# Performance work log

Measured on AMD Instinct MI355X. Metric: run time of the kernel, lower is better.

Reference implementation:

```python
import jax, jax.numpy as jnp
import numpy as np

B, C, N = 512, 4, 24
D, H, L, DFF = 512, 8, 4, 2048
D2, D4 = D // 2, D // 4


def _ln(x, g, b):
    m = x.mean(-1, keepdims=True)
    v = ((x - m) ** 2).mean(-1, keepdims=True)
    return (x - m) / jnp.sqrt(v + 1e-5) * g + b


def setup_inputs():
    key = jax.random.key(0)
    ks = iter(jax.random.split(key, 80))
    def glorot(shape):
        fi, fo = shape[-2], shape[-1]
        return jax.random.normal(next(ks), shape, jnp.float32) * np.float32(np.sqrt(2.0 / (fi + fo)))
    z = lambda shape: jnp.zeros(shape, jnp.float32)
    o = lambda shape: jnp.ones(shape, jnp.float32)
    inp = {
        'encoded_features': jax.random.normal(next(ks), (B, C, D), jnp.float32),
        'original_keypoints': jax.random.normal(next(ks), (B, C, N, 2), jnp.float32),
        'depth_map': jax.random.uniform(next(ks), (B, C, N), jnp.float32),
        'occlusion_mask': jax.random.bernoulli(next(ks), 0.7, (B, C, N)),
        'kp_emb': jax.random.normal(next(ks), (N, D), jnp.float32) * 0.02,
        'view_emb': jax.random.normal(next(ks), (C, D), jnp.float32) * 0.02,
        'Wq': glorot((L, D, D)), 'bq': z((L, D)),
        'Wk': glorot((L, D, D)), 'bk': z((L, D)),
        'Wv': glorot((L, D, D)), 'bv': z((L, D)),
        'Wo': glorot((L, D, D)), 'bo': z((L, D)),
        'ln1_g': o((L, D)), 'ln1_b': z((L, D)),
        'ln2_g': o((L, D)), 'ln2_b': z((L, D)),
        'ffn_w1': glorot((L, D, DFF)), 'ffn_b1': z((L, DFF)),
        'ffn_w2': glorot((L, DFF, D)), 'ffn_b2': z((L, D)),
        'pred_w1': glorot((D, D2)), 'pred_b1': z((D2,)),
        'pred_w2': glorot((D2, D4)), 'pred_b2': z((D4,)),
        'pred_w3': glorot((D4, 2)), 'pred_b3': z((2,)),
        'de_w1': glorot((1, D4)), 'de_b1': z((D4,)),
        'de_w2': glorot((D4, D2)), 'de_b2': z((D2,)),
        'mp_w': glorot((D + D2, D)), 'mp_b': z((D,)),
        'dp_w1': glorot((D, D2)), 'dp_b1': z((D2,)),
        'dp_w2': glorot((D2, D4)), 'dp_b2': z((D4,)),
        'dp_w3': glorot((D4, 1)), 'dp_b3': z((1,)),
        'conf_w': glorot((D, 1)), 'conf_b': z((1,)),
    }
    return inp


def _forward(encoded_features, original_keypoints, depth_map, kp_emb, view_emb,
             Wq, bq, Wk, bk, Wv, bv, Wo, bo, ln1_g, ln1_b, ln2_g, ln2_b,
             ffn_w1, ffn_b1, ffn_w2, ffn_b2, pred_w1, pred_b1, pred_w2, pred_b2,
             pred_w3, pred_b3, de_w1, de_b1, de_w2, de_b2, mp_w, mp_b,
             dp_w1, dp_b1, dp_w2, dp_b2, dp_w3, dp_b3, conf_w, conf_b,
             occlusion_mask):
    occluded = ~occlusion_mask  # (B,C,N) True = needs inpainting
    # Vectorized replacement for the nested B*C ragged depth loop:
    # encode every depth scalar, masked mean over visible keypoints per (b,c).
    d_enc = jax.nn.gelu(depth_map[..., None] @ de_w1 + de_b1) @ de_w2 + de_b2  # (B,C,N,D2)
    vis = occlusion_mask[..., None].astype(jnp.float32)
    cnt = vis.sum(2)  # (B,C,1)
    depth_feat = jnp.where(cnt > 0, (d_enc * vis).sum(2) / jnp.maximum(cnt, 1.0), 0.0)
    # NOTE: faithful to source — `memory` is projected but the attention layers
    # consume encoded_features directly, so this is dead w.r.t. outputs.
    _memory = jnp.concatenate([encoded_features, depth_feat], -1) @ mp_w + mp_b

    # Dense query set over all (c,n); occluded positions selected at the end
    # (same math as the nonzero/gather version, jit-friendly fixed shapes).
    q = (view_emb[:, None, :] + kp_emb[None, :, :]).reshape(1, C * N, D)
    q = jnp.broadcast_to(q, (B, C * N, D))
    mem = encoded_features  # (B,C,D)
    dh = D // H
    scale = np.float32(1.0 / np.sqrt(dh))
    for l in range(L):  # post-LN cross-attention block (assumed standard block)
        qh = (q @ Wq[l] + bq[l]).reshape(B, C * N, H, dh)
        kh = (mem @ Wk[l] + bk[l]).reshape(B, C, H, dh)
        vh = (mem @ Wv[l] + bv[l]).reshape(B, C, H, dh)
        att = jax.nn.softmax(jnp.einsum('bqhd,bkhd->bhqk', qh, kh) * scale, axis=-1)
        attn_out = jnp.einsum('bhqk,bkhd->bqhd', att, vh).reshape(B, C * N, D) @ Wo[l] + bo[l]
        q = _ln(q + attn_out, ln1_g[l], ln1_b[l])
        f = jax.nn.gelu(q @ ffn_w1[l] + ffn_b1[l]) @ ffn_w2[l] + ffn_b2[l]
        q = _ln(q + f, ln2_g[l], ln2_b[l])

    feat = q  # (B, C*N, D)
    pred = jax.nn.gelu(feat @ pred_w1 + pred_b1)
    pred = jax.nn.gelu(pred @ pred_w2 + pred_b2) @ pred_w3 + pred_b3  # (B,CN,2)
    coords = jnp.where(occluded[..., None], pred.reshape(B, C, N, 2), original_keypoints)
    conf = jnp.where(occluded, jax.nn.sigmoid(feat @ conf_w + conf_b).reshape(B, C, N), 0.0)
    dp = jax.nn.gelu(feat @ dp_w1 + dp_b1)
    dp = jax.nn.softplus(jax.nn.gelu(dp @ dp_w2 + dp_b2) @ dp_w3 + dp_b3)
    depth = jnp.where(occluded, dp.reshape(B, C, N), 0.0)
    return coords, conf, depth


def reference(encoded_features, original_keypoints, depth_map, kp_emb, view_emb,
              Wq, bq, Wk, bk, Wv, bv, Wo, bo, ln1_g, ln1_b, ln2_g, ln2_b,
              ffn_w1, ffn_b1, ffn_w2, ffn_b2, pred_w1, pred_b1, pred_w2, pred_b2,
              pred_w3, pred_b3, de_w1, de_b1, de_w2, de_b2, mp_w, mp_b,
              dp_w1, dp_b1, dp_w2, dp_b2, dp_w3, dp_b3, conf_w, conf_b,
              occlusion_mask):
    return _forward(encoded_features, original_keypoints, depth_map, kp_emb, view_emb,
                    Wq, bq, Wk, bk, Wv, bv, Wo, bo, ln1_g, ln1_b, ln2_g, ln2_b,
                    ffn_w1, ffn_b1, ffn_w2, ffn_b2, pred_w1, pred_b1, pred_w2, pred_b2,
                    pred_w3, pred_b3, de_w1, de_b1, de_w2, de_b2, mp_w, mp_b,
                    dp_w1, dp_b1, dp_w2, dp_b2, dp_w3, dp_b3, conf_w, conf_b,
                    occlusion_mask)
```

## Files before the change

kernel.cpp:

```cpp
#include <hip/hip_runtime.h>
#include <hip/hip_bf16.h>
#include <stdint.h>

using bf16 = __hip_bfloat16;
typedef __attribute__((ext_vector_type(8))) short short8;
typedef __attribute__((ext_vector_type(4))) float f32x4;

#define GLD16(gptr, lptr) \
  __builtin_amdgcn_global_load_lds((const __attribute__((address_space(1))) void*)(gptr), \
                                   (__attribute__((address_space(3))) void*)(lptr), 16, 0, 0)

__device__ __forceinline__ float b2f(bf16 h){ return __bfloat162float(h); }
__device__ __forceinline__ bf16  f2b(float f){ return __float2bfloat16(f); }
__device__ __forceinline__ float geluf(float x){
  float t2 = 1.5957691216057308f * (x + 0.044715f*x*x*x);
  return x / (1.0f + __expf(-t2));
}
__device__ __forceinline__ float wsum(float v){
  v += __shfl_xor(v,32); v += __shfl_xor(v,16); v += __shfl_xor(v,8);
  v += __shfl_xor(v,4);  v += __shfl_xor(v,2);  v += __shfl_xor(v,1);
  return v;
}

union BV { uint4 u; bf16 h[8]; };

template<int EPI>
__global__ __launch_bounds__(256, 4)
void gemm_bt(const bf16* __restrict__ A, int lda,
             const bf16* __restrict__ Bt,
             const float* __restrict__ bias,
             bf16* __restrict__ C, int ldc, int K)
{
  __shared__ __align__(16) bf16 smem[17408];
  const int tid  = threadIdx.x;
  const int wave = tid >> 6;
  const int lane = tid & 63;

  const int nwg = gridDim.x * gridDim.y;
  int bid = blockIdx.x + gridDim.x * blockIdx.y;
  if ((nwg & 7) == 0) bid = (bid & 7) * (nwg >> 3) + (bid >> 3);
  const int bx = bid % gridDim.x;
  const int by = bid / gridDim.x;
  const long mBlk = (long)by * 128;
  const int  nBlk = bx * 128;
  const int wm = (wave >> 1) * 64;
  const int wn = (wave & 1)  * 64;

  const int lr = lane >> 3;
  const int kc = ((lane & 7) ^ lr) << 3;
  const bf16* aS = A  + (mBlk + wave*32 + lr) * (long)lda + kc;
  const bf16* bS = Bt + (long)(nBlk + wave*32 + lr) * K   + kc;

  const int sA = lane >> 4;
  const int rA = wm + (lane & 15);
  const int rB = wn + (lane & 15);
  const int xA = rA & 7, xB = rB & 7;

  f32x4 acc[4][4];
  #pragma unroll
  for (int m=0;m<4;++m)
    #pragma unroll
    for (int n=0;n<4;++n)
      acc[m][n] = (f32x4){0.f,0.f,0.f,0.f};

  const int nt = K >> 6;
  for (int t = 0; t < nt; ++t) {
    {
      bf16* sAl = smem + wave*2048;
      bf16* sBl = smem + 8192 + wave*2048;
      const int ko = t*64;
      #pragma unroll
      for (int c=0;c<4;++c) {
        GLD16(aS + (long)c*8*lda + ko, sAl + c*512);
        GLD16(bS + (long)c*8*K   + ko, sBl + c*512);
      }
    }
    __syncthreads();
    #pragma unroll
    for (int ks=0; ks<2; ++ks) {
      const int j = (ks<<2) + sA;
      short8 af[4], bfv[4];
      #pragma unroll
      for (int m=0;m<4;++m)
        af[m]  = *(const short8*)&smem[(rA + m*16)*64 + ((j ^ xA) << 3)];
      #pragma unroll
      for (int n=0;n<4;++n)
        bfv[n] = *(const short8*)&smem[8192 + (rB + n*16)*64 + ((j ^ xB) << 3)];
      #pragma unroll
      for (int m=0;m<4;++m)
        #pragma unroll
        for (int n=0;n<4;++n)
          acc[m][n] = __builtin_amdgcn_mfma_f32_16x16x32_bf16(af[m], bfv[n], acc[m][n], 0, 0, 0);
    }
    __syncthreads();
  }

  #pragma unroll
  for (int n=0;n<4;++n) {
    const int col = wn + n*16 + (lane & 15);
    float bi = bias[nBlk + col];
    #pragma unroll
    for (int m=0;m<4;++m) {
      #pragma unroll
      for (int j=0;j<4;++j) {
        float x = acc[m][n][j] + bi;
        if (EPI == 1) x = geluf(x);
        smem[(wm + m*16 + (lane>>4)*4 + j)*136 + col] = f2b(x);
      }
    }
  }
  __syncthreads();
  #pragma unroll
  for (int it=0; it<8; ++it) {
    int o = it*2048 + tid*8;
    int row = o >> 7, col = o & 127;
    uint4 v = *(const uint4*)&smem[row*136 + col];
    *(uint4*)&C[(mBlk + row)*(long)ldc + nBlk + col] = v;
  }
}

__global__ void transpose_w(const float* __restrict__ src, bf16* __restrict__ dst,
                            int N, long srcStride, long dstStride, int dstRowOff, int dstLd)
{
  __shared__ float t[32][33];
  src += (long)blockIdx.z * srcStride;
  dst += (long)blockIdx.z * dstStride;
  int n0 = blockIdx.x*32, k0 = blockIdx.y*32;
  int tx = threadIdx.x & 31, ty = threadIdx.x >> 5;
  #pragma unroll
  for (int r=0;r<4;++r) t[ty + r*8][tx] = src[(long)(k0+ty+r*8)*N + n0+tx];
  __syncthreads();
  #pragma unroll
  for (int r=0;r<4;++r)
    dst[(long)(dstRowOff + n0 + ty + r*8)*dstLd + k0 + tx] = f2b(t[tx][ty+r*8]);
}

__global__ void f32_to_bf16_k(const float* __restrict__ src, bf16* __restrict__ dst, long n)
{
  long i = ((long)blockIdx.x*256 + threadIdx.x) * 4;
  if (i + 3 < n) {
    float4 v = *(const float4*)(src + i);
    dst[i+0]=f2b(v.x); dst[i+1]=f2b(v.y); dst[i+2]=f2b(v.z); dst[i+3]=f2b(v.w);
  }
}

__global__ void concat2(float* __restrict__ dst, long dStride,
                        const float* __restrict__ a, long aStride, int na,
                        const float* __restrict__ b, long bStride, int nb)
{
  int z = blockIdx.y;
  int i = blockIdx.x*256 + threadIdx.x;
  if (i < na) dst[z*dStride + i] = a[z*aStride + i];
  else if (i < na + nb) dst[z*dStride + i] = b[z*bStride + (i - na)];
}

__global__ void init_q(const float* __restrict__ vw, const float* __restrict__ kp,
                       bf16* __restrict__ q)
{
  long gid = (long)blockIdx.x*256 + threadIdx.x;
  int b  = (int)(gid / 6144);
  int r  = (int)(gid % 6144);
  int cn = r >> 6;
  int d0 = (r & 63) * 8;
  int c = cn / 24, n = cn % 24;
  const float4* v4 = (const float4*)(vw + c*512 + d0);
  const float4* k4 = (const float4*)(kp + n*512 + d0);
  float4 va = v4[0], vb = v4[1], ka = k4[0], kb = k4[1];
  BV o;
  o.h[0]=f2b(va.x+ka.x); o.h[1]=f2b(va.y+ka.y); o.h[2]=f2b(va.z+ka.z); o.h[3]=f2b(va.w+ka.w);
  o.h[4]=f2b(vb.x+kb.x); o.h[5]=f2b(vb.y+kb.y); o.h[6]=f2b(vb.z+kb.z); o.h[7]=f2b(vb.w+kb.w);
  *(uint4*)(q + (long)b*49152 + cn*512 + d0) = o.u;
}

__global__ void init_q96(const float* __restrict__ vw, const float* __restrict__ kp,
                         bf16* __restrict__ q96)
{
  int gid = blockIdx.x*256 + threadIdx.x;
  int cn = gid >> 6;
  int d0 = (gid & 63) * 8;
  int c = cn / 24, n = cn % 24;
  const float4* v4 = (const float4*)(vw + c*512 + d0);
  const float4* k4 = (const float4*)(kp + n*512 + d0);
  float4 va = v4[0], vb = v4[1], ka = k4[0], kb = k4[1];
  BV o;
  o.h[0]=f2b(va.x+ka.x); o.h[1]=f2b(va.y+ka.y); o.h[2]=f2b(va.z+ka.z); o.h[3]=f2b(va.w+ka.w);
  o.h[4]=f2b(vb.x+kb.x); o.h[5]=f2b(vb.y+kb.y); o.h[6]=f2b(vb.z+kb.z); o.h[7]=f2b(vb.w+kb.w);
  *(uint4*)(q96 + (long)cn*512 + d0) = o.u;
}

__global__ void add_ln(bf16* __restrict__ q, const bf16* __restrict__ res,
                       const float* __restrict__ g, const float* __restrict__ b)
{
  int row  = blockIdx.x*4 + (threadIdx.x >> 6);
  int lane = threadIdx.x & 63;
  long o = (long)row*512 + lane*8;
  BV Q, R;
  Q.u = *(const uint4*)(q + o);
  R.u = *(const uint4*)(res + o);
  float s[8]; float sum=0.f, sq=0.f;
  #pragma unroll
  for (int j=0;j<8;++j){ s[j] = b2f(Q.h[j]) + b2f(R.h[j]); sum += s[j]; sq += s[j]*s[j]; }
  sum = wsum(sum); sq = wsum(sq);
  float mean = sum * 0.001953125f;
  float var  = sq  * 0.001953125f - mean*mean;
  float rstd = rsqrtf(var + 1e-5f);
  const float4* g4 = (const float4*)(g + lane*8);
  const float4* b4 = (const float4*)(b + lane*8);
  float4 g0=g4[0], g1=g4[1], b0=b4[0], b1=b4[1];
  float gg[8] = {g0.x,g0.y,g0.z,g0.w,g1.x,g1.y,g1.z,g1.w};
  float bb[8] = {b0.x,b0.y,b0.z,b0.w,b1.x,b1.y,b1.z,b1.w};
  BV O;
  #pragma unroll
  for (int j=0;j<8;++j) O.h[j] = f2b((s[j]-mean)*rstd*gg[j] + bb[j]);
  *(uint4*)(q + o) = O.u;
}

__global__ void attn_k(const bf16* __restrict__ qsrc, int qMod,
                       const bf16* __restrict__ kvh, bf16* __restrict__ dst)
{
  int row  = blockIdx.x*4 + (threadIdx.x >> 6);
  int lane = threadIdx.x & 63;
  int b = row / 96;
  int qRow = qMod ? (row % qMod) : row;
  int d = (lane >> 3)*64 + (lane & 7)*8;
  BV Q;
  Q.u = *(const uint4*)(qsrc + (long)qRow*512 + d);
  float qf[8];
  #pragma unroll
  for (int j=0;j<8;++j) qf[j] = b2f(Q.h[j]);
  float s[4];
  #pragma unroll
  for (int c=0;c<4;++c){
    BV K; K.u = *(const uint4*)(kvh + (long)(b*4+c)*1024 + d);
    float p = 0.f;
    #pragma unroll
    for (int j=0;j<8;++j) p += qf[j]*b2f(K.h[j]);
    p += __shfl_xor(p,1); p += __shfl_xor(p,2); p += __shfl_xor(p,4);
    s[c] = p * 0.125f;
  }
  float mx = fmaxf(fmaxf(s[0],s[1]), fmaxf(s[2],s[3]));
  float e0=expf(s[0]-mx), e1=expf(s[1]-mx), e2=expf(s[2]-mx), e3=expf(s[3]-mx);
  float inv = 1.f/(e0+e1+e2+e3);
  float p4[4] = {e0*inv, e1*inv, e2*inv, e3*inv};
  float o[8] = {0,0,0,0,0,0,0,0};
  #pragma unroll
  for (int c=0;c<4;++c){
    BV V; V.u = *(const uint4*)(kvh + (long)(b*4+c)*1024 + 512 + d);
    #pragma unroll
    for (int j=0;j<8;++j) o[j] += p4[c]*b2f(V.h[j]);
  }
  BV O;
  #pragma unroll
  for (int j=0;j<8;++j) O.h[j] = f2b(o[j]);
  *(uint4*)(dst + (long)row*512 + d) = O.u;
}

__global__ void finalize_k(const bf16* __restrict__ feat, const bf16* __restrict__ p2dp2,
                           const float* __restrict__ cw, const float* __restrict__ cb,
                           const float* __restrict__ pw3, const float* __restrict__ pb3,
                           const float* __restrict__ dw3, const float* __restrict__ db3,
                           const int* __restrict__ occ, const float* __restrict__ okp,
                           float* __restrict__ out)
{
  int row  = blockIdx.x*4 + (threadIdx.x >> 6);
  int lane = threadIdx.x & 63;
  BV F; F.u = *(const uint4*)(feat + (long)row*512 + lane*8);
  const float4* c4 = (const float4*)(cw + lane*8);
  float4 ca = c4[0], cbv = c4[1];
  float cwv[8] = {ca.x,ca.y,ca.z,ca.w,cbv.x,cbv.y,cbv.z,cbv.w};
  float pc = 0.f;
  #pragma unroll
  for (int j=0;j<8;++j) pc += b2f(F.h[j]) * cwv[j];
  float sc = wsum(pc);
  int k = lane*2;
  long o2 = (long)row*256;
  float a0 = b2f(p2dp2[o2 + k]),       a1 = b2f(p2dp2[o2 + k + 1]);
  float d0 = b2f(p2dp2[o2 + 128 + k]), d1 = b2f(p2dp2[o2 + 128 + k + 1]);
  float sx = a0*pw3[k*2]   + a1*pw3[(k+1)*2];
  float sy = a0*pw3[k*2+1] + a1*pw3[(k+1)*2+1];
  float sd = d0*dw3[k]     + d1*dw3[k+1];
  sx = wsum(sx); sy = wsum(sy); sd = wsum(sd);
  if (lane == 0) {
    bool occl = (occ[row] == 0);
    out[row*2]   = occl ? (sx + pb3[0]) : okp[row*2];
    out[row*2+1] = occl ? (sy + pb3[1]) : okp[row*2+1];
    out[98304 + row] = occl ? 1.f/(1.f + expf(-(sc + cb[0]))) : 0.f;
    float dd = sd + db3[0];
    float sp = fmaxf(dd, 0.f) + log1pf(expf(-fabsf(dd)));
    out[147456 + row] = occl ? sp : 0.f;
  }
}

extern "C" void kernel_launch(void* const* d_in, const int* in_sizes, int n_in,
                              void* d_out, int out_size, void* d_ws, size_t ws_size,
                              hipStream_t stream)
{
  const float* enc  = (const float*)d_in[0];
  const float* okp  = (const float*)d_in[1];
  const int*   occ  = (const int*)  d_in[3];
  const float* kp   = (const float*)d_in[4];
  const float* vw   = (const float*)d_in[5];
  const float* Wq   = (const float*)d_in[6];
  const float* bq   = (const float*)d_in[7];
  const float* Wk   = (const float*)d_in[8];
  const float* bk   = (const float*)d_in[9];
  const float* Wv   = (const float*)d_in[10];
  const float* bv   = (const float*)d_in[11];
  const float* Wo   = (const float*)d_in[12];
  const float* bo   = (const float*)d_in[13];
  const float* ln1g = (const float*)d_in[14];
  const float* ln1b = (const float*)d_in[15];
  const float* ln2g = (const float*)d_in[16];
  const float* ln2b = (const float*)d_in[17];
  const float* fw1  = (const float*)d_in[18];
  const float* fb1  = (const float*)d_in[19];
  const float* fw2  = (const float*)d_in[20];
  const float* fb2  = (const float*)d_in[21];
  const float* pw1  = (const float*)d_in[22];
  const float* pb1  = (const float*)d_in[23];
  const float* pw2  = (const float*)d_in[24];
  const float* pb2  = (const float*)d_in[25];
  const float* pw3  = (const float*)d_in[26];
  const float* pb3  = (const float*)d_in[27];
  const float* dw1  = (const float*)d_in[34];
  const float* db1  = (const float*)d_in[35];
  const float* dw2  = (const float*)d_in[36];
  const float* db2  = (const float*)d_in[37];
  const float* dw3  = (const float*)d_in[38];
  const float* db3  = (const float*)d_in[39];
  const float* cw   = (const float*)d_in[40];
  const float* cb   = (const float*)d_in[41];

  uint8_t* base = (uint8_t*)d_ws;
  size_t off = 0;
  auto alloc = [&](size_t bytes) -> void* {
    void* p = base + off;
    off = (off + bytes + 255) & ~(size_t)255;
    return p;
  };
  bf16*  wqT  = (bf16*) alloc(4ull*512*512*2);
  bf16*  kvT  = (bf16*) alloc(4ull*1024*512*2);
  bf16*  woT  = (bf16*) alloc(4ull*512*512*2);
  bf16*  w1T  = (bf16*) alloc(4ull*2048*512*2);
  bf16*  w2T  = (bf16*) alloc(4ull*512*2048*2);
  bf16*  pd1T = (bf16*) alloc(512ull*512*2);
  bf16*  pw2T = (bf16*) alloc(128ull*256*2);
  bf16*  dw2T = (bf16*) alloc(128ull*256*2);
  float* bkvb = (float*)alloc(4ull*1024*4);
  float* pd1b = (float*)alloc(512ull*4);
  bf16*  mem16= (bf16*) alloc(2048ull*512*2);
  bf16*  kv16 = (bf16*) alloc(2048ull*1024*2);
  bf16*  q96  = (bf16*) alloc(128ull*512*2);
  bf16*  qh96 = (bf16*) alloc(128ull*512*2);
  bf16*  q16  = (bf16*) alloc(49152ull*512*2);
  bf16*  bufQH= (bf16*) alloc(49152ull*512*2);
  size_t remainB = (ws_size > off) ? (ws_size - off) : 0;
  int chunkRows;
  if      (remainB >= 16384ull*2048*2 + 512) chunkRows = 16384;
  else if (remainB >= 12288ull*2048*2 + 512) chunkRows = 12288;
  else                                        chunkRows = 6144;
  bf16*  bufF1= (bf16*) alloc((size_t)chunkRows*2048*2);
  if (off > ws_size) return;
  const int nCh = 49152 / chunkRows;
  long woRows = (long)chunkRows * 4;
  if (woRows > 49152) woRows = 49152;
  const int nWo = (int)(49152 / woRows);

  dim3 T(256);
  transpose_w<<<dim3(16,16,4), T, 0, stream>>>(Wq,  wqT, 512, 512*512, 512*512, 0, 512);
  transpose_w<<<dim3(16,16,4), T, 0, stream>>>(Wk,  kvT, 512, 512*512, 1024*512, 0, 512);
  transpose_w<<<dim3(16,16,4), T, 0, stream>>>(Wv,  kvT, 512, 512*512, 1024*512, 512, 512);
  transpose_w<<<dim3(16,16,4), T, 0, stream>>>(Wo,  woT, 512, 512*512, 512*512, 0, 512);
  transpose_w<<<dim3(64,16,4), T, 0, stream>>>(fw1, w1T, 2048, 512*2048, 2048*512, 0, 512);
  transpose_w<<<dim3(16,64,4), T, 0, stream>>>(fw2, w2T, 512, 2048*512, 512*2048, 0, 2048);
  transpose_w<<<dim3(8,16,1),  T, 0, stream>>>(pw1, pd1T, 256, 0, 0, 0,   512);
  transpose_w<<<dim3(8,16,1),  T, 0, stream>>>(dw1, pd1T, 256, 0, 0, 256, 512);
  transpose_w<<<dim3(4,8,1),   T, 0, stream>>>(pw2, pw2T, 128, 0, 0, 0, 256);
  transpose_w<<<dim3(4,8,1),   T, 0, stream>>>(dw2, dw2T, 128, 0, 0, 0, 256);
  concat2<<<dim3(4,4), T, 0, stream>>>(bkvb, 1024, bk, 512, 512, bv, 512, 512);
  concat2<<<dim3(2,1), T, 0, stream>>>(pd1b, 512, pb1, 256, 256, db1, 256, 256);
  f32_to_bf16_k<<<dim3(1024), T, 0, stream>>>(enc, mem16, 2048ll*512);
  init_q<<<dim3(12288), T, 0, stream>>>(vw, kp, q16);
  init_q96<<<dim3(24), T, 0, stream>>>(vw, kp, q96);

  for (int l = 0; l < 4; ++l) {
    if (l == 0) {
      gemm_bt<0><<<dim3(4,1), T, 0, stream>>>(q96, 512, wqT, bq, qh96, 512, 512);
    } else {
      gemm_bt<0><<<dim3(4,384), T, 0, stream>>>(q16, 512, wqT + l*262144, bq + l*512, bufQH, 512, 512);
    }
    gemm_bt<0><<<dim3(8,16),  T, 0, stream>>>(mem16, 512, kvT + l*524288, bkvb + l*1024, kv16, 1024, 512);
    if (l == 0) attn_k<<<dim3(12288), T, 0, stream>>>(qh96, 96, kv16, bufQH);
    else        attn_k<<<dim3(12288), T, 0, stream>>>(bufQH, 0, kv16, bufQH);
    for (int c = 0; c < nWo; ++c) {
      gemm_bt<0><<<dim3(4, (int)(woRows>>7)), T, 0, stream>>>(bufQH + (long)c*woRows*512, 512,
                                                woT + l*262144, bo + l*512, bufF1, 512, 512);
      add_ln<<<dim3((int)(woRows>>2)), T, 0, stream>>>(q16 + (long)c*woRows*512, bufF1,
                                           ln1g + l*512, ln1b + l*512);
    }
    for (int c = 0; c < nCh; ++c) {
      gemm_bt<1><<<dim3(16, chunkRows>>7), T, 0, stream>>>(q16 + (long)c*chunkRows*512, 512,
                                                w1T + l*1048576, fb1 + l*2048, bufF1, 2048, 512);
      gemm_bt<0><<<dim3(4, chunkRows>>7),  T, 0, stream>>>(bufF1, 2048,
                                                w2T + l*1048576, fb2 + l*512,
                                                bufQH + (long)c*chunkRows*512, 512, 2048);
      add_ln<<<dim3(chunkRows>>2), T, 0, stream>>>(q16 + (long)c*chunkRows*512,
                                           bufQH + (long)c*chunkRows*512,
                                           ln2g + l*512, ln2b + l*512);
    }
  }

  gemm_bt<1><<<dim3(4,384), T, 0, stream>>>(q16, 512, pd1T, pd1b, bufQH, 512, 512);
  gemm_bt<1><<<dim3(1,384), T, 0, stream>>>(bufQH, 512, pw2T, pb2, bufF1, 256, 256);
  gemm_bt<1><<<dim3(1,384), T, 0, stream>>>(bufQH + 256, 512, dw2T, db2, bufF1 + 128, 256, 256);
  finalize_k<<<dim3(12288), T, 0, stream>>>(q16, bufF1, cw, cb, pw3, pb3, dw3, db3,
                                            occ, okp, (float*)d_out);
}
```

Before: 1.653 ms.

## Give each wave a private double-buffered LDS tile to drop block barriers

Changes the GEMM main loop so each wave loads its own A and B rows into a private, double-buffered LDS region with K-step 32. Global-to-LDS loads are issued two stages ahead and ordered with explicit vmcnt/lgkmcnt waits instead of __syncthreads, so loads overlap MFMA work. The bias load is hoisted before the loop. LDS use grows to 64KB and launch bounds drop to 2 blocks per CU, which lowers occupancy. Each wave now loads its operand rows redundantly rather than sharing them across the block, which adds global and LDS traffic.

```diff
diff --git a/kernel.cpp b/kernel.cpp
--- a/kernel.cpp
+++ b/kernel.cpp
@@ -25,13 +25,13 @@
 union BV { uint4 u; bf16 h[8]; };
 
 template<int EPI>
-__global__ __launch_bounds__(256, 4)
+__global__ __launch_bounds__(256, 2)
 void gemm_bt(const bf16* __restrict__ A, int lda,
              const bf16* __restrict__ Bt,
              const float* __restrict__ bias,
              bf16* __restrict__ C, int ldc, int K)
 {
-  __shared__ __align__(16) bf16 smem[17408];
+  __shared__ __align__(16) bf16 smem[32768];
   const int tid  = threadIdx.x;
   const int wave = tid >> 6;
   const int lane = tid & 63;
@@ -46,15 +46,20 @@
   const int wm = (wave >> 1) * 64;
   const int wn = (wave & 1)  * 64;
 
-  const int lr = lane >> 3;
-  const int kc = ((lane & 7) ^ lr) << 3;
-  const bf16* aS = A  + (mBlk + wave*32 + lr) * (long)lda + kc;
-  const bf16* bS = Bt + (long)(nBlk + wave*32 + lr) * K   + kc;
+  const int srow  = lane >> 2;
+  const int schunk = (lane & 3) ^ ((lane >> 3) & 3);
+  const bf16* aS = A  + (mBlk + wm + srow) * (long)lda + schunk*8;
+  const bf16* bS = Bt + (long)(nBlk + wn + srow) * K   + schunk*8;
+  bf16* const wbase = smem + wave*8192;
 
   const int sA = lane >> 4;
-  const int rA = wm + (lane & 15);
-  const int rB = wn + (lane & 15);
-  const int xA = rA & 7, xB = rB & 7;
+  const int frA = lane & 15;
+
+  float bi[4];
+  #pragma unroll
+  for (int n=0;n<4;++n) bi[n] = bias[nBlk + wn + n*16 + (lane & 15)];
+  asm volatile("s_waitcnt vmcnt(0)" ::: "memory");
+  asm volatile("" : "+v"(bi[0]), "+v"(bi[1]), "+v"(bi[2]), "+v"(bi[3]));
 
   f32x4 acc[4][4];
   #pragma unroll
@@ -63,47 +68,60 @@
     for (int n=0;n<4;++n)
       acc[m][n] = (f32x4){0.f,0.f,0.f,0.f};
 
-  const int nt = K >> 6;
-  for (int t = 0; t < nt; ++t) {
-    {
-      bf16* sAl = smem + wave*2048;
-      bf16* sBl = smem + 8192 + wave*2048;
-      const int ko = t*64;
-      #pragma unroll
-      for (int c=0;c<4;++c) {
-        GLD16(aS + (long)c*8*lda + ko, sAl + c*512);
-        GLD16(bS + (long)c*8*K   + ko, sBl + c*512);
-      }
-    }
-    __syncthreads();
-    #pragma unroll
-    for (int ks=0; ks<2; ++ks) {
-      const int j = (ks<<2) + sA;
-      short8 af[4], bfv[4];
-      #pragma unroll
-      for (int m=0;m<4;++m)
-        af[m]  = *(const short8*)&smem[(rA + m*16)*64 + ((j ^ xA) << 3)];
+  auto STAGE = [&](int buf, int t) {
+    bf16* sAl = wbase + buf*4096;
+    bf16* sBl = wbase + buf*4096 + 2048;
+    const int ko = t*32;
+    #pragma unroll
+    for (int c=0;c<4;++c) {
+      GLD16(aS + (long)c*16*lda + ko, sAl + c*512);
+      GLD16(bS + (long)c*16*K   + ko, sBl + c*512);
+    }
+  };
+  auto COMPUTE = [&](int buf) {
+    const bf16* s = wbase + buf*4096;
+    short8 af[4], bfv[4];
+    #pragma unroll
+    for (int m=0;m<4;++m) {
+      const int r = frA + m*16;
+      af[m]  = *(const short8*)&s[r*32 + ((sA ^ ((r>>1)&3)) << 3)];
+    }
+    #pragma unroll
+    for (int n=0;n<4;++n) {
+      const int r = frA + n*16;
+      bfv[n] = *(const short8*)&s[2048 + r*32 + ((sA ^ ((r>>1)&3)) << 3)];
+    }
+    #pragma unroll
+    for (int m=0;m<4;++m)
       #pragma unroll
       for (int n=0;n<4;++n)
-        bfv[n] = *(const short8*)&smem[8192 + (rB + n*16)*64 + ((j ^ xB) << 3)];
-      #pragma unroll
-      for (int m=0;m<4;++m)
-        #pragma unroll
-        for (int n=0;n<4;++n)
-          acc[m][n] = __builtin_amdgcn_mfma_f32_16x16x32_bf16(af[m], bfv[n], acc[m][n], 0, 0, 0);
-    }
-    __syncthreads();
-  }
-
+        acc[m][n] = __builtin_amdgcn_mfma_f32_16x16x32_bf16(af[m], bfv[n], acc[m][n], 0, 0, 0);
+  };
+
+  STAGE(0, 0);
+  STAGE(1, 1);
+
+  const int nt = K >> 5;
+  for (int t = 0; t < nt - 2; ++t) {
+    asm volatile("s_waitcnt vmcnt(8)" ::: "memory");
+    COMPUTE(t & 1);
+    asm volatile("s_waitcnt lgkmcnt(0)" ::: "memory");
+    STAGE(t & 1, t + 2);
+  }
+  asm volatile("s_waitcnt vmcnt(8)" ::: "memory");
+  COMPUTE(nt & 1);
+  asm volatile("s_waitcnt vmcnt(0)" ::: "memory");
+  COMPUTE((nt & 1) ^ 1);
+
+  __syncthreads();
   #pragma unroll
   for (int n=0;n<4;++n) {
     const int col = wn + n*16 + (lane & 15);
-    float bi = bias[nBlk + col];
     #pragma unroll
     for (int m=0;m<4;++m) {
       #pragma unroll
       for (int j=0;j<4;++j) {
-        float x = acc[m][n][j] + bi;
+        float x = acc[m][n][j] + bi[n];
         if (EPI == 1) x = geluf(x);
         smem[(wm + m*16 + (lane>>4)*4 + j)*136 + col] = f2b(x);
       }
```

New measurement: 2.171 ms. 1.31x slower.
